# Kernel optimization log

Measured on AMD Instinct MI355X. Metric: run time of the kernel, lower is better.

The kernel has to match this reference:

```python
import jax, jax.numpy as jnp
import numpy as np

N_HEADS = 4

def setup_inputs() -> dict:
    key = jax.random.key(0)
    ks = jax.random.split(key, 11)
    B, HW, C = 4, 4096, 256
    d = dict(
        q_in=jax.random.normal(ks[0], (B, HW, C), jnp.float32),
        k_in=jax.random.normal(ks[1], (B, HW, C), jnp.float32),
        v_in=jax.random.normal(ks[2], (B, HW, C), jnp.float32),
        wq=jax.random.normal(ks[3], (C,), jnp.float32),
        bq=jax.random.normal(ks[4], (C,), jnp.float32),
        wk=jax.random.normal(ks[5], (C,), jnp.float32),
        bk=jax.random.normal(ks[6], (C,), jnp.float32),
        wv=jax.random.normal(ks[7], (C,), jnp.float32),
        bv=jax.random.normal(ks[8], (C,), jnp.float32),
        wp=jax.random.normal(ks[9], (C,), jnp.float32),
        bp=jax.random.normal(ks[10], (C,), jnp.float32),
    )
    return d


def reference(q_in, k_in, v_in, wq, bq, wk, bk, wv, bv, wp, bp):
    # depthwise 1x1 grouped convs (groups == channels) == per-channel scale + bias
    q = q_in * wq + bq            # (B, HW, C)
    k = k_in * wk + bk
    v = v_in * wv + bv
    B, HW, C = q.shape
    d = C // N_HEADS
    scale = float(d) ** -0.5
    q = q.reshape(B, HW, N_HEADS, d).transpose(0, 2, 1, 3)  # (B, H, HW, d)
    k = k.reshape(B, HW, N_HEADS, d).transpose(0, 2, 1, 3)
    v = v.reshape(B, HW, N_HEADS, d).transpose(0, 2, 1, 3)
    att = jax.nn.softmax(jnp.einsum('bhqd,bhkd->bhqk', q, k) * scale, axis=-1)
    out = jnp.einsum('bhqk,bhkd->bhqd', att, v)             # (B, H, HW, d)
    out = out.transpose(0, 2, 1, 3).reshape(B, HW, C)       # (B, HW, C)
    return out * wp + bp
```

## Files before the change

### kernel.cpp

```cpp
#include <hip/hip_runtime.h>


#define HW 4096
#define CCH 256
#define DH 64
#define NH 4
#define QTILE 256
#define KTILE 64
#define LOG2E 1.44269504088896340736f

typedef __attribute__((ext_vector_type(8))) _Float16 half8;
typedef __attribute__((ext_vector_type(4))) _Float16 half4;
typedef __attribute__((ext_vector_type(2))) __fp16 pk16x2;
typedef __attribute__((ext_vector_type(4))) float floatx4;

typedef __attribute__((address_space(1))) const unsigned int gbl_u32;
typedef __attribute__((address_space(3))) unsigned int lds_u32;

__device__ __forceinline__ void gload_lds16(const void* g, void* l) {
    __builtin_amdgcn_global_load_lds((gbl_u32*)g, (lds_u32*)l, 16, 0, 0);
}
__device__ __forceinline__ floatx4 mfma_k32(half8 a, half8 b, floatx4 c) {
    return __builtin_amdgcn_mfma_f32_16x16x32_f16(a, b, c, 0, 0, 0);
}

__global__ __launch_bounds__(256) void prepass_all(
    const float* __restrict__ q_in, const float* __restrict__ k_in,
    const float* __restrict__ v_in,
    const float* __restrict__ wq, const float* __restrict__ bq,
    const float* __restrict__ wk, const float* __restrict__ bk,
    const float* __restrict__ wv, const float* __restrict__ bv,
    _Float16* __restrict__ Qhat, _Float16* __restrict__ Khat,
    _Float16* __restrict__ Vthat)
{
    if (blockIdx.x < 4096) {
        int idx = (blockIdx.x * 256 + threadIdx.x) * 4;
        int b = idx >> 20;
        int rem = idx & ((1 << 20) - 1);
        int row = rem >> 8;
        int c = rem & 255;
        int h = c >> 6;
        int ch = c & 63;
        floatx4 q4 = *(const floatx4*)(q_in + idx);
        floatx4 k4 = *(const floatx4*)(k_in + idx);
        floatx4 wq4 = *(const floatx4*)(wq + c);
        floatx4 bq4 = *(const floatx4*)(bq + c);
        floatx4 wk4 = *(const floatx4*)(wk + c);
        floatx4 bk4 = *(const floatx4*)(bk + c);
        const float qsc = 0.125f * LOG2E;
        half4 qh, kh;
        qh[0] = (_Float16)((q4.x * wq4.x + bq4.x) * qsc);
        qh[1] = (_Float16)((q4.y * wq4.y + bq4.y) * qsc);
        qh[2] = (_Float16)((q4.z * wq4.z + bq4.z) * qsc);
        qh[3] = (_Float16)((q4.w * wq4.w + bq4.w) * qsc);
        kh[0] = (_Float16)(k4.x * wk4.x + bk4.x);
        kh[1] = (_Float16)(k4.y * wk4.y + bk4.y);
        kh[2] = (_Float16)(k4.z * wk4.z + bk4.z);
        kh[3] = (_Float16)(k4.w * wk4.w + bk4.w);
        size_t o_q = ((size_t)(b * NH + h) * HW + row) * DH + ch;
        int p = row & 31;
        int srow = ((p & 4) << 2) + ((p >> 3) << 2) + (p & 3);
        int row_k = (row & ~31) | srow;
        size_t o_k = ((size_t)(b * NH + h) * HW + row_k) * DH + ch;
        *(half4*)(Qhat + o_q) = qh;
        *(half4*)(Khat + o_k) = kh;
    } else {
        __shared__ _Float16 Lt[64 * 68];
        int bx = blockIdx.x - 4096;
        int t = threadIdx.x;
        int key0 = (bx & 63) * 64;
        int bh = bx >> 6;
        int b = bh >> 2, h = bh & 3;
        int c4 = (t & 15) * 4;
        floatx4 wv4 = *(const floatx4*)(wv + h * DH + c4);
        floatx4 bv4 = *(const floatx4*)(bv + h * DH + c4);
        #pragma unroll
        for (int p = 0; p < 4; ++p) {
            int key = p * 16 + (t >> 4);
            const float* vp = v_in + ((size_t)b * HW + key0 + key) * CCH + h * DH + c4;
            floatx4 v4 = *(const floatx4*)vp;
            half4 vh;
            vh[0] = (_Float16)(v4.x * wv4.x + bv4.x);
            vh[1] = (_Float16)(v4.y * wv4.y + bv4.y);
            vh[2] = (_Float16)(v4.z * wv4.z + bv4.z);
            vh[3] = (_Float16)(v4.w * wv4.w + bv4.w);
            *(half4*)(&Lt[key * 68 + c4]) = vh;
        }
        __syncthreads();
        #pragma unroll
        for (int p = 0; p < 2; ++p) {
            int ch = p * 32 + (t >> 3);
            int kg = (t & 7) * 8;
            half8 v8;
            #pragma unroll
            for (int j = 0; j < 8; ++j) v8[j] = Lt[(kg + j) * 68 + ch];
            *(half8*)(Vthat + ((size_t)bh * DH + ch) * HW + key0 + kg) = v8;
        }
    }
}

__launch_bounds__(512, 2)
__global__ void attn_kernel(
    const _Float16* __restrict__ Qhat, const _Float16* __restrict__ Khat,
    const _Float16* __restrict__ Vthat,
    const float* __restrict__ wp, const float* __restrict__ bp,
    float* __restrict__ out)
{
    __shared__ alignas(16) char pool[131072];

    const int tid = threadIdx.x;
    const int wave = tid >> 6;
    const int lane = tid & 63;
    const int l15 = lane & 15;
    const int quad = lane >> 4;
    const int ksw = l15 & 7;
    const int qw = wave & 3;
    const int par = wave >> 2;

    const int f = blockIdx.x;
    const int xcd = f & 7;
    const int s = f >> 3;
    const int bh = 2 * xcd + (s >> 4);
    const int qtile = s & 15;

    const int q0 = qtile * QTILE + qw * 64;
    half8 qfrag[4][2];
    #pragma unroll
    for (int g = 0; g < 4; ++g) {
        const _Float16* qp = Qhat + ((size_t)bh * HW + q0 + g * 16 + l15) * DH + quad * 8;
        qfrag[g][0] = *(const half8*)(qp);
        qfrag[g][1] = *(const half8*)(qp + 32);
    }

    const int srow0 = lane >> 3;
    const int sw = (lane & 7) ^ srow0;
    const _Float16* kgp = Khat + ((size_t)bh * HW + wave * 8 + srow0) * DH + sw * 8;
    const _Float16* vgp = Vthat + ((size_t)bh * DH + wave * 8 + srow0) * HW + sw * 8;

    half8 ones8;
    #pragma unroll
    for (int j = 0; j < 8; ++j) ones8[j] = (_Float16)1.0f;

    floatx4 acc[4][4];
    floatx4 accl[4];
    #pragma unroll
    for (int g = 0; g < 4; ++g) {
        floatx4 z = {0.f,0.f,0.f,0.f};
        accl[g] = z;
        #pragma unroll
        for (int nt = 0; nt < 4; ++nt) acc[g][nt] = z;
    }

    half8 kf[4][2];

    #define STAGE(st, SP) do {                                                 \
        const size_t koff = (size_t)(st) * 128 * DH;                           \
        const size_t voff = (size_t)(st) * 128;                                \
        gload_lds16(kgp + koff,           (SP) + wave * 1024);                 \
        gload_lds16(kgp + koff + 64 * DH, (SP) + 8192 + wave * 1024);          \
        gload_lds16(vgp + voff,           (SP) + 16384 + wave * 1024);         \
        gload_lds16(vgp + voff + 64,      (SP) + 24576 + wave * 1024);         \
    } while (0)

    #define LOADK(SP) do {                                                     \
        const _Float16* KBn = (const _Float16*)((SP) + par * 8192);            \
        _Pragma("unroll")                                                      \
        for (int kt = 0; kt < 4; ++kt) {                                       \
            const _Float16* kr = KBn + (l15 + 16 * kt) * 64;                   \
            kf[kt][0] = *(const half8*)(kr + ((quad ^ ksw) * 8));              \
            kf[kt][1] = *(const half8*)(kr + (((4 + quad) ^ ksw) * 8));        \
        }                                                                      \
    } while (0)

    #define HALF_TILE(c, VB) do {                                              \
        half8 pfrag[4];                                                        \
        __builtin_amdgcn_s_setprio(1);                                         \
        _Pragma("unroll")                                                      \
        for (int g = 0; g < 4; ++g) {                                          \
            floatx4 sa = {-8.f,-8.f,-8.f,-8.f};                                \
            floatx4 sb = sa;                                                   \
            sa = mfma_k32(kf[2*(c)][0], qfrag[g][0], sa);                      \
            sa = mfma_k32(kf[2*(c)][1], qfrag[g][1], sa);                      \
            sb = mfma_k32(kf[2*(c)+1][0], qfrag[g][0], sb);                    \
            sb = mfma_k32(kf[2*(c)+1][1], qfrag[g][1], sb);                    \
            float a0 = __builtin_amdgcn_exp2f(sa[0]);                          \
            float a1 = __builtin_amdgcn_exp2f(sa[1]);                          \
            float a2 = __builtin_amdgcn_exp2f(sa[2]);                          \
            float a3 = __builtin_amdgcn_exp2f(sa[3]);                          \
            float b0 = __builtin_amdgcn_exp2f(sb[0]);                          \
            float b1 = __builtin_amdgcn_exp2f(sb[1]);                          \
            float b2 = __builtin_amdgcn_exp2f(sb[2]);                          \
            float b3 = __builtin_amdgcn_exp2f(sb[3]);                          \
            pk16x2 p01 = __builtin_amdgcn_cvt_pkrtz(a0, a1);                   \
            pk16x2 p23 = __builtin_amdgcn_cvt_pkrtz(a2, a3);                   \
            pk16x2 p45 = __builtin_amdgcn_cvt_pkrtz(b0, b1);                   \
            pk16x2 p67 = __builtin_amdgcn_cvt_pkrtz(b2, b3);                   \
            half8 pk;                                                          \
            pk[0] = (_Float16)p01[0]; pk[1] = (_Float16)p01[1];                \
            pk[2] = (_Float16)p23[0]; pk[3] = (_Float16)p23[1];                \
            pk[4] = (_Float16)p45[0]; pk[5] = (_Float16)p45[1];                \
            pk[6] = (_Float16)p67[0]; pk[7] = (_Float16)p67[1];                \
            pfrag[g] = pk;                                                     \
        }                                                                      \
        _Pragma("unroll")                                                      \
        for (int g = 0; g < 4; ++g)                                            \
            accl[g] = mfma_k32(ones8, pfrag[g], accl[g]);                      \
        _Pragma("unroll")                                                      \
        for (int nt = 0; nt < 4; ++nt) {                                       \
            const _Float16* vr = (VB) + (l15 + 16 * nt) * 64                   \
                + ((((c) * 4 + quad) ^ ksw) * 8);                              \
            half8 vf = *(const half8*)vr;                                      \
            _Pragma("unroll")                                                  \
            for (int g = 0; g < 4; ++g)                                        \
                acc[g][nt] = mfma_k32(vf, pfrag[g], acc[g][nt]);               \
        }                                                                      \
        __builtin_amdgcn_s_setprio(0);                                         \
    } while (0)

    #define COMPUTE(SPcur, SPnext, DO_NEXT) do {                               \
        const _Float16* VB = (const _Float16*)((SPcur) + 16384 + par * 8192);  \
        HALF_TILE(0, VB);                                                      \
        {                                                                      \
            half8 pfrag[4];                                                    \
            __builtin_amdgcn_s_setprio(1);                                     \
            _Pragma("unroll")                                                  \
            for (int g = 0; g < 4; ++g) {                                      \
                floatx4 sa = {-8.f,-8.f,-8.f,-8.f};                            \
                floatx4 sb = sa;                                               \
                sa = mfma_k32(kf[2][0], qfrag[g][0], sa);                      \
                sa = mfma_k32(kf[2][1], qfrag[g][1], sa);                      \
                sb = mfma_k32(kf[3][0], qfrag[g][0], sb);                      \
                sb = mfma_k32(kf[3][1], qfrag[g][1], sb);                      \
                float a0 = __builtin_amdgcn_exp2f(sa[0]);                      \
                float a1 = __builtin_amdgcn_exp2f(sa[1]);                      \
                float a2 = __builtin_amdgcn_exp2f(sa[2]);                      \
                float a3 = __builtin_amdgcn_exp2f(sa[3]);                      \
                float b0 = __builtin_amdgcn_exp2f(sb[0]);                      \
                float b1 = __builtin_amdgcn_exp2f(sb[1]);                      \
                float b2 = __builtin_amdgcn_exp2f(sb[2]);                      \
                float b3 = __builtin_amdgcn_exp2f(sb[3]);                      \
                pk16x2 p01 = __builtin_amdgcn_cvt_pkrtz(a0, a1);               \
                pk16x2 p23 = __builtin_amdgcn_cvt_pkrtz(a2, a3);               \
                pk16x2 p45 = __builtin_amdgcn_cvt_pkrtz(b0, b1);               \
                pk16x2 p67 = __builtin_amdgcn_cvt_pkrtz(b2, b3);               \
                half8 pk;                                                      \
                pk[0] = (_Float16)p01[0]; pk[1] = (_Float16)p01[1];            \
                pk[2] = (_Float16)p23[0]; pk[3] = (_Float16)p23[1];            \
                pk[4] = (_Float16)p45[0]; pk[5] = (_Float16)p45[1];            \
                pk[6] = (_Float16)p67[0]; pk[7] = (_Float16)p67[1];            \
                pfrag[g] = pk;                                                 \
            }                                                                  \
            __builtin_amdgcn_s_setprio(0);                                     \
            if (DO_NEXT) LOADK(SPnext);     \
            __builtin_amdgcn_s_setprio(1);                                     \
            _Pragma("unroll")                                                  \
            for (int g = 0; g < 4; ++g)                                        \
                accl[g] = mfma_k32(ones8, pfrag[g], accl[g]);                  \
            _Pragma("unroll")                                                  \
            for (int nt = 0; nt < 4; ++nt) {                                   \
                const _Float16* vr = VB + (l15 + 16 * nt) * 64                 \
                    + (((4 + quad) ^ ksw) * 8);                                \
                half8 vf = *(const half8*)vr;                                  \
                _Pragma("unroll")                                              \
                for (int g = 0; g < 4; ++g)                                    \
                    acc[g][nt] = mfma_k32(vf, pfrag[g], acc[g][nt]);           \
            }                                                                  \
            __builtin_amdgcn_s_setprio(0);                                     \
        }                                                                      \
    } while (0)

    #define WAITVM(n) asm volatile("s_waitcnt vmcnt(" #n ")" ::: "memory")
    #define BARS() do { __builtin_amdgcn_s_barrier();                          \
                        __builtin_amdgcn_sched_barrier(0); } while (0)

    char* set0 = pool;
    char* set1 = pool + 32768;
    char* set2 = pool + 65536;
    char* set3 = pool + 98304;

    STAGE(0, set0);
    STAGE(1, set1);
    STAGE(2, set2);
    WAITVM(8); BARS();
    LOADK(set0);
    for (int t = 0; t < 28; t += 4) {
        WAITVM(4); BARS(); STAGE(t + 3, set3); COMPUTE(set0, set1, 1);
        WAITVM(4); BARS(); STAGE(t + 4, set0); COMPUTE(set1, set2, 1);
        WAITVM(4); BARS(); STAGE(t + 5, set1); COMPUTE(set2, set3, 1);
        WAITVM(4); BARS(); STAGE(t + 6, set2); COMPUTE(set3, set0, 1);
    }
    WAITVM(4); BARS(); STAGE(31, set3); COMPUTE(set0, set1, 1);
    WAITVM(4); BARS(); COMPUTE(set1, set2, 1);
    WAITVM(0); BARS(); COMPUTE(set2, set3, 1);
    COMPUTE(set3, set0, 0);

    const int b = bh >> 2, h = bh & 3, ch0 = h * DH;
    float* P1 = (float*)pool;
    float* Pl = (float*)(pool + 69632);

    __syncthreads();
    if (par == 1) {
        #pragma unroll
        for (int g = 0; g < 4; ++g) {
            #pragma unroll
            for (int nt = 0; nt < 4; ++nt)
                *(floatx4*)&P1[qw * 4352 + (g * 16 + l15) * 68 + nt * 16 + quad * 4] = acc[g][nt];
            if (quad == 0) {
                Pl[qw * 64 + g * 16 + l15] = accl[g][0];
            }
        }
    }
    __syncthreads();
    if (par == 0) {
        #pragma unroll
        for (int g = 0; g < 4; ++g) {
            float lB = Pl[qw * 64 + g * 16 + l15];
            float inv = 1.0f / (accl[g][0] + lB);
            #pragma unroll
            for (int nt = 0; nt < 4; ++nt) {
                floatx4 vB = *(const floatx4*)&P1[qw * 4352 + (g * 16 + l15) * 68 + nt * 16 + quad * 4];
                #pragma unroll
                for (int r = 0; r < 4; ++r)
                    acc[g][nt][r] = (acc[g][nt][r] + vB[r]) * inv;
            }
        }
    }
    __syncthreads();
    if (par == 0) {
        floatx4 wp4 = *(const floatx4*)(wp + ch0 + l15 * 4);
        floatx4 bp4 = *(const floatx4*)(bp + ch0 + l15 * 4);
        float* Ot = (float*)(pool) + qw * 2304;
        #pragma unroll
        for (int p = 0; p < 2; ++p) {
            #pragma unroll
            for (int gg = 0; gg < 2; ++gg) {
                int g = p * 2 + gg;
                #pragma unroll
                for (int nt = 0; nt < 4; ++nt)
                    *(floatx4*)&Ot[(gg * 16 + l15) * 72 + nt * 16 + quad * 4] = acc[g][nt];
            }
            #pragma unroll
            for (int i = 0; i < 8; ++i) {
                int q = i * 4 + quad;
                floatx4 v = *(const floatx4*)&Ot[q * 72 + l15 * 4];
                floatx4 o;
                o.x = v.x * wp4.x + bp4.x;
                o.y = v.y * wp4.y + bp4.y;
                o.z = v.z * wp4.z + bp4.z;
                o.w = v.w * wp4.w + bp4.w;
                *(floatx4*)(out + ((size_t)b * HW + q0 + p * 32 + q) * CCH + ch0 + l15 * 4) = o;
            }
        }
    }
    #undef STAGE
    #undef LOADK
    #undef HALF_TILE
    #undef COMPUTE
    #undef WAITVM
    #undef BARS
}

extern "C" void kernel_launch(void* const* d_in, const int* in_sizes, int n_in,
                              void* d_out, int out_size, void* d_ws, size_t ws_size,
                              hipStream_t stream) {
    const float* q_in = (const float*)d_in[0];
    const float* k_in = (const float*)d_in[1];
    const float* v_in = (const float*)d_in[2];
    const float* wq = (const float*)d_in[3];
    const float* bq = (const float*)d_in[4];
    const float* wk = (const float*)d_in[5];
    const float* bk = (const float*)d_in[6];
    const float* wv = (const float*)d_in[7];
    const float* bv = (const float*)d_in[8];
    const float* wp = (const float*)d_in[9];
    const float* bp = (const float*)d_in[10];
    float* out = (float*)d_out;

    const size_t tensor_halves = (size_t)4 * NH * HW * DH;
    _Float16* Qhat = (_Float16*)d_ws;
    _Float16* Khat = Qhat + tensor_halves;
    _Float16* Vthat = Khat + tensor_halves;

    prepass_all<<<dim3(4096 + 1024), 256, 0, stream>>>(
        q_in, k_in, v_in, wq, bq, wk, bk, wv, bv, Qhat, Khat, Vthat);
    attn_kernel<<<dim3(HW / QTILE * 4 * NH), 512, 0, stream>>>(
        Qhat, Khat, Vthat, wp, bp, out);
}
```

Measured before the change: 82.43 us.

## Compute softmax row sums in VALU and stagger wave schedules by parity

```diff
diff --git a/kernel.cpp b/kernel.cpp
--- a/kernel.cpp
+++ b/kernel.cpp
@@ -137,16 +137,12 @@
     const _Float16* kgp = Khat + ((size_t)bh * HW + wave * 8 + srow0) * DH + sw * 8;
     const _Float16* vgp = Vthat + ((size_t)bh * DH + wave * 8 + srow0) * HW + sw * 8;
 
-    half8 ones8;
-    #pragma unroll
-    for (int j = 0; j < 8; ++j) ones8[j] = (_Float16)1.0f;
-
     floatx4 acc[4][4];
-    floatx4 accl[4];
+    float accl_s[4];
     #pragma unroll
     for (int g = 0; g < 4; ++g) {
+        accl_s[g] = 0.0f;
         floatx4 z = {0.f,0.f,0.f,0.f};
-        accl[g] = z;
         #pragma unroll
         for (int nt = 0; nt < 4; ++nt) acc[g][nt] = z;
     }
@@ -172,17 +168,16 @@
         }                                                                      \
     } while (0)
 
-    #define HALF_TILE(c, VB) do {                                              \
-        half8 pfrag[4];                                                        \
+    #define GENH(cc, pf) do {                                                  \
         __builtin_amdgcn_s_setprio(1);                                         \
         _Pragma("unroll")                                                      \
         for (int g = 0; g < 4; ++g) {                                          \
             floatx4 sa = {-8.f,-8.f,-8.f,-8.f};                                \
             floatx4 sb = sa;                                                   \
-            sa = mfma_k32(kf[2*(c)][0], qfrag[g][0], sa);                      \
-            sa = mfma_k32(kf[2*(c)][1], qfrag[g][1], sa);                      \
-            sb = mfma_k32(kf[2*(c)+1][0], qfrag[g][0], sb);                    \
-            sb = mfma_k32(kf[2*(c)+1][1], qfrag[g][1], sb);                    \
+            sa = mfma_k32(kf[2*(cc)][0], qfrag[g][0], sa);                     \
+            sa = mfma_k32(kf[2*(cc)][1], qfrag[g][1], sa);                     \
+            sb = mfma_k32(kf[2*(cc)+1][0], qfrag[g][0], sb);                   \
+            sb = mfma_k32(kf[2*(cc)+1][1], qfrag[g][1], sb);                   \
             float a0 = __builtin_amdgcn_exp2f(sa[0]);                          \
             float a1 = __builtin_amdgcn_exp2f(sa[1]);                          \
             float a2 = __builtin_amdgcn_exp2f(sa[2]);                          \
@@ -191,6 +186,7 @@
             float b1 = __builtin_amdgcn_exp2f(sb[1]);                          \
             float b2 = __builtin_amdgcn_exp2f(sb[2]);                          \
             float b3 = __builtin_amdgcn_exp2f(sb[3]);                          \
+            accl_s[g] += ((a0 + a1) + (a2 + a3)) + ((b0 + b1) + (b2 + b3));    \
             pk16x2 p01 = __builtin_amdgcn_cvt_pkrtz(a0, a1);                   \
             pk16x2 p23 = __builtin_amdgcn_cvt_pkrtz(a2, a3);                   \
             pk16x2 p45 = __builtin_amdgcn_cvt_pkrtz(b0, b1);                   \
@@ -200,72 +196,42 @@
             pk[2] = (_Float16)p23[0]; pk[3] = (_Float16)p23[1];                \
             pk[4] = (_Float16)p45[0]; pk[5] = (_Float16)p45[1];                \
             pk[6] = (_Float16)p67[0]; pk[7] = (_Float16)p67[1];                \
-            pfrag[g] = pk;                                                     \
+            pf[g] = pk;                                                        \
         }                                                                      \
-        _Pragma("unroll")                                                      \
-        for (int g = 0; g < 4; ++g)                                            \
-            accl[g] = mfma_k32(ones8, pfrag[g], accl[g]);                      \
+        __builtin_amdgcn_s_setprio(0);                                         \
+    } while (0)
+
+    #define PVH(cc, pf, VB) do {                                               \
+        __builtin_amdgcn_s_setprio(1);                                         \
         _Pragma("unroll")                                                      \
         for (int nt = 0; nt < 4; ++nt) {                                       \
             const _Float16* vr = (VB) + (l15 + 16 * nt) * 64                   \
-                + ((((c) * 4 + quad) ^ ksw) * 8);                              \
+                + ((((cc) * 4 + quad) ^ ksw) * 8);                             \
             half8 vf = *(const half8*)vr;                                      \
             _Pragma("unroll")                                                  \
             for (int g = 0; g < 4; ++g)                                        \
-                acc[g][nt] = mfma_k32(vf, pfrag[g], acc[g][nt]);               \
+                acc[g][nt] = mfma_k32(vf, pf[g], acc[g][nt]);                  \
         }                                                                      \
         __builtin_amdgcn_s_setprio(0);                                         \
     } while (0)
 
     #define COMPUTE(SPcur, SPnext, DO_NEXT) do {                               \
         const _Float16* VB = (const _Float16*)((SPcur) + 16384 + par * 8192);  \
-        HALF_TILE(0, VB);                                                      \
-        {                                                                      \
-            half8 pfrag[4];                                                    \
-            __builtin_amdgcn_s_setprio(1);                                     \
-            _Pragma("unroll")                                                  \
-            for (int g = 0; g < 4; ++g) {                                      \
-                floatx4 sa = {-8.f,-8.f,-8.f,-8.f};                            \
-                floatx4 sb = sa;                                               \
-                sa = mfma_k32(kf[2][0], qfrag[g][0], sa);                      \
-                sa = mfma_k32(kf[2][1], qfrag[g][1], sa);                      \
-                sb = mfma_k32(kf[3][0], qfrag[g][0], sb);                      \
-                sb = mfma_k32(kf[3][1], qfrag[g][1], sb);                      \
-                float a0 = __builtin_amdgcn_exp2f(sa[0]);                      \
-                float a1 = __builtin_amdgcn_exp2f(sa[1]);                      \
-                float a2 = __builtin_amdgcn_exp2f(sa[2]);                      \
-                float a3 = __builtin_amdgcn_exp2f(sa[3]);                      \
-                float b0 = __builtin_amdgcn_exp2f(sb[0]);                      \
-                float b1 = __builtin_amdgcn_exp2f(sb[1]);                      \
-                float b2 = __builtin_amdgcn_exp2f(sb[2]);                      \
-                float b3 = __builtin_amdgcn_exp2f(sb[3]);                      \
-                pk16x2 p01 = __builtin_amdgcn_cvt_pkrtz(a0, a1);               \
-                pk16x2 p23 = __builtin_amdgcn_cvt_pkrtz(a2, a3);               \
-                pk16x2 p45 = __builtin_amdgcn_cvt_pkrtz(b0, b1);               \
-                pk16x2 p67 = __builtin_amdgcn_cvt_pkrtz(b2, b3);               \
-                half8 pk;                                                      \
-                pk[0] = (_Float16)p01[0]; pk[1] = (_Float16)p01[1];            \
-                pk[2] = (_Float16)p23[0]; pk[3] = (_Float16)p23[1];            \
-                pk[4] = (_Float16)p45[0]; pk[5] = (_Float16)p45[1];            \
-                pk[6] = (_Float16)p67[0]; pk[7] = (_Float16)p67[1];            \
-                pfrag[g] = pk;                                                 \
-            }                                                                  \
-            __builtin_amdgcn_s_setprio(0);                                     \
-            if (DO_NEXT) LOADK(SPnext);     \
-            __builtin_amdgcn_s_setprio(1);                                     \
-            _Pragma("unroll")                                                  \
-            for (int g = 0; g < 4; ++g)                                        \
-                accl[g] = mfma_k32(ones8, pfrag[g], accl[g]);                  \
-            _Pragma("unroll")                                                  \
-            for (int nt = 0; nt < 4; ++nt) {                                   \
-                const _Float16* vr = VB + (l15 + 16 * nt) * 64                 \
-                    + (((4 + quad) ^ ksw) * 8);                                \
-                half8 vf = *(const half8*)vr;                                  \
-                _Pragma("unroll")                                              \
-                for (int g = 0; g < 4; ++g)                                    \
-                    acc[g][nt] = mfma_k32(vf, pfrag[g], acc[g][nt]);           \
-            }                                                                  \
-            __builtin_amdgcn_s_setprio(0);                                     \
+        if (par) {                                                             \
+            half8 pf0[4], pf1[4];                                              \
+            GENH(0, pf0);                                                      \
+            GENH(1, pf1);                                                      \
+            if (DO_NEXT) LOADK(SPnext);                                        \
+            PVH(0, pf0, VB);                                                   \
+            PVH(1, pf1, VB);                                                   \
+        } else {                                                               \
+            half8 pf0[4];                                                      \
+            GENH(0, pf0);                                                      \
+            PVH(0, pf0, VB);                                                   \
+            half8 pf1[4];                                                      \
+            GENH(1, pf1);                                                      \
+            if (DO_NEXT) LOADK(SPnext);                                        \
+            PVH(1, pf1, VB);                                                   \
         }                                                                      \
     } while (0)
 
@@ -294,6 +260,12 @@
     WAITVM(0); BARS(); COMPUTE(set2, set3, 1);
     COMPUTE(set3, set0, 0);
 
+    #pragma unroll
+    for (int g = 0; g < 4; ++g) {
+        accl_s[g] += __shfl_xor(accl_s[g], 16);
+        accl_s[g] += __shfl_xor(accl_s[g], 32);
+    }
+
     const int b = bh >> 2, h = bh & 3, ch0 = h * DH;
     float* P1 = (float*)pool;
     float* Pl = (float*)(pool + 69632);
@@ -306,7 +278,7 @@
             for (int nt = 0; nt < 4; ++nt)
                 *(floatx4*)&P1[qw * 4352 + (g * 16 + l15) * 68 + nt * 16 + quad * 4] = acc[g][nt];
             if (quad == 0) {
-                Pl[qw * 64 + g * 16 + l15] = accl[g][0];
+                Pl[qw * 64 + g * 16 + l15] = accl_s[g];
             }
         }
     }
@@ -315,7 +287,7 @@
         #pragma unroll
         for (int g = 0; g < 4; ++g) {
             float lB = Pl[qw * 64 + g * 16 + l15];
-            float inv = 1.0f / (accl[g][0] + lB);
+            float inv = 1.0f / (accl_s[g] + lB);
             #pragma unroll
             for (int nt = 0; nt < 4; ++nt) {
                 floatx4 vB = *(const floatx4*)&P1[qw * 4352 + (g * 16 + l15) * 68 + nt * 16 + quad * 4];
@@ -354,7 +326,8 @@
     }
     #undef STAGE
     #undef LOADK
-    #undef HALF_TILE
+    #undef GENH
+    #undef PVH
     #undef COMPUTE
     #undef WAITVM
     #undef BARS
```

After: 88.89 us. 7.8% more time.

## Load K fragments directly from global into registers, stage only V in LDS

Applied to the files above, without the earlier changes.

```diff
diff --git a/kernel.cpp b/kernel.cpp
--- a/kernel.cpp
+++ b/kernel.cpp
@@ -106,7 +106,7 @@
     const float* __restrict__ wp, const float* __restrict__ bp,
     float* __restrict__ out)
 {
-    __shared__ alignas(16) char pool[131072];
+    __shared__ alignas(16) char pool[73728];
 
     const int tid = threadIdx.x;
     const int wave = tid >> 6;
@@ -134,8 +134,9 @@
 
     const int srow0 = lane >> 3;
     const int sw = (lane & 7) ^ srow0;
-    const _Float16* kgp = Khat + ((size_t)bh * HW + wave * 8 + srow0) * DH + sw * 8;
     const _Float16* vgp = Vthat + ((size_t)bh * DH + wave * 8 + srow0) * HW + sw * 8;
+
+    const _Float16* kbase = Khat + ((size_t)bh * HW + par * 64 + l15) * DH + quad * 8;
 
     half8 ones8;
     #pragma unroll
@@ -154,21 +155,17 @@
     half8 kf[4][2];
 
     #define STAGE(st, SP) do {                                                 \
-        const size_t koff = (size_t)(st) * 128 * DH;                           \
         const size_t voff = (size_t)(st) * 128;                                \
-        gload_lds16(kgp + koff,           (SP) + wave * 1024);                 \
-        gload_lds16(kgp + koff + 64 * DH, (SP) + 8192 + wave * 1024);          \
-        gload_lds16(vgp + voff,           (SP) + 16384 + wave * 1024);         \
-        gload_lds16(vgp + voff + 64,      (SP) + 24576 + wave * 1024);         \
+        gload_lds16(vgp + voff,      (SP) + wave * 1024);                      \
+        gload_lds16(vgp + voff + 64, (SP) + 8192 + wave * 1024);               \
     } while (0)
 
-    #define LOADK(SP) do {                                                     \
-        const _Float16* KBn = (const _Float16*)((SP) + par * 8192);            \
+    #define LOADK(st) do {                                                     \
+        const _Float16* Kb = kbase + (size_t)(st) * 128 * DH;                  \
         _Pragma("unroll")                                                      \
         for (int kt = 0; kt < 4; ++kt) {                                       \
-            const _Float16* kr = KBn + (l15 + 16 * kt) * 64;                   \
-            kf[kt][0] = *(const half8*)(kr + ((quad ^ ksw) * 8));              \
-            kf[kt][1] = *(const half8*)(kr + (((4 + quad) ^ ksw) * 8));        \
+            kf[kt][0] = *(const half8*)(Kb + kt * 16 * DH);                    \
+            kf[kt][1] = *(const half8*)(Kb + kt * 16 * DH + 32);               \
         }                                                                      \
     } while (0)
 
@@ -217,8 +214,8 @@
         __builtin_amdgcn_s_setprio(0);                                         \
     } while (0)
 
-    #define COMPUTE(SPcur, SPnext, DO_NEXT) do {                               \
-        const _Float16* VB = (const _Float16*)((SPcur) + 16384 + par * 8192);  \
+    #define COMPUTE(SPcur, nextst, DO_NEXT) do {                               \
+        const _Float16* VB = (const _Float16*)((SPcur) + par * 8192);          \
         HALF_TILE(0, VB);                                                      \
         {                                                                      \
             half8 pfrag[4];                                                    \
@@ -251,7 +248,7 @@
                 pfrag[g] = pk;                                                 \
             }                                                                  \
             __builtin_amdgcn_s_setprio(0);                                     \
-            if (DO_NEXT) LOADK(SPnext);     \
+            if (DO_NEXT) LOADK(nextst);     \
             __builtin_amdgcn_s_setprio(1);                                     \
             _Pragma("unroll")                                                  \
             for (int g = 0; g < 4; ++g)                                        \
@@ -274,25 +271,26 @@
                         __builtin_amdgcn_sched_barrier(0); } while (0)
 
     char* set0 = pool;
-    char* set1 = pool + 32768;
-    char* set2 = pool + 65536;
-    char* set3 = pool + 98304;
+    char* set1 = pool + 16384;
+    char* set2 = pool + 32768;
+    char* set3 = pool + 49152;
 
     STAGE(0, set0);
     STAGE(1, set1);
     STAGE(2, set2);
-    WAITVM(8); BARS();
-    LOADK(set0);
-    for (int t = 0; t < 28; t += 4) {
-        WAITVM(4); BARS(); STAGE(t + 3, set3); COMPUTE(set0, set1, 1);
-        WAITVM(4); BARS(); STAGE(t + 4, set0); COMPUTE(set1, set2, 1);
-        WAITVM(4); BARS(); STAGE(t + 5, set1); COMPUTE(set2, set3, 1);
-        WAITVM(4); BARS(); STAGE(t + 6, set2); COMPUTE(set3, set0, 1);
-    }
-    WAITVM(4); BARS(); STAGE(31, set3); COMPUTE(set0, set1, 1);
-    WAITVM(4); BARS(); COMPUTE(set1, set2, 1);
-    WAITVM(0); BARS(); COMPUTE(set2, set3, 1);
-    COMPUTE(set3, set0, 0);
+    LOADK(0);
+    WAITVM(12); BARS();
+    STAGE(3, set3);
+    COMPUTE(set0, 1, 1);
+    for (int t = 1; t <= 25; t += 4) {
+        WAITVM(10); BARS(); STAGE(t + 3, set0); COMPUTE(set1, t + 1, 1);
+        WAITVM(10); BARS(); STAGE(t + 4, set1); COMPUTE(set2, t + 2, 1);
+        WAITVM(10); BARS(); STAGE(t + 5, set2); COMPUTE(set3, t + 3, 1);
+        WAITVM(10); BARS(); STAGE(t + 6, set3); COMPUTE(set0, t + 4, 1);
+    }
+    WAITVM(10); BARS(); COMPUTE(set1, 30, 1);
+    WAITVM(8);  BARS(); COMPUTE(set2, 31, 1);
+    WAITVM(8);  BARS(); COMPUTE(set3, 0, 0);
 
     const int b = bh >> 2, h = bh & 3, ch0 = h * DH;
     float* P1 = (float*)pool;
```

Measured after the change: 111.0 us. 1.35x slower.
